# Optimization experiments

Measured on AMD Instinct MI355X. Metric: run time of the kernel, lower is better.

Reference implementation:

```python
import jax, jax.numpy as jnp
import numpy as np
import math

EPS = 1e-5
L2_EPS = 1e-12  # torch F.normalize default eps


def _bitlinear(x, W):
    """BitNet b1.58-style BitLinear: ternary weights (per-tensor mean-abs scale)
    and per-token int8 absmax activation quantization. No bias.
    x: [..., in], W: [out, in] -> [..., out]
    """
    w_scale = jnp.clip(jnp.mean(jnp.abs(W)), EPS, None)
    W_q = jnp.clip(jnp.round(W / w_scale), -1.0, 1.0) * w_scale
    x_scale = 127.0 / jnp.clip(jnp.max(jnp.abs(x), axis=-1, keepdims=True), EPS, None)
    x_q = jnp.clip(jnp.round(x * x_scale), -128.0, 127.0) / x_scale
    return jnp.einsum('bsi,oi->bso', x_q, W_q)


def setup_inputs() -> dict:
    key = jax.random.key(0)
    k1, k2, k3 = jax.random.split(key, 3)
    B, S, D_in, P, D_out = 4, 4096, 2048, 16, 2048
    x = jax.random.normal(k1, (B, S, D_in), dtype=jnp.float32)
    # xavier_normal_: std = sqrt(2 / (fan_in + fan_out))
    Wk = jax.random.normal(k2, (P, D_in), dtype=jnp.float32) * math.sqrt(2.0 / (D_in + P))
    Wv = jax.random.normal(k3, (D_out, P), dtype=jnp.float32) * math.sqrt(2.0 / (P + D_out))
    return {"x": x, "Wk": Wk, "Wv": Wv}


def reference(x, Wk, Wv):
    # key projection -> [B, S, P]
    attn = _bitlinear(x, Wk)
    # gelu (exact erf form, torch default) + L2-normalize * sqrt(P)
    attn = jax.nn.gelu(attn, approximate=False)
    norm = jnp.clip(jnp.linalg.norm(attn, axis=-1, keepdims=True), L2_EPS, None)
    attn = attn / norm * jnp.sqrt(jnp.float32(attn.shape[-1]))
    # value projection -> [B, S, D_out]
    return _bitlinear(attn, Wv)
```

## Files before the change

kernel.cpp:

```cpp
#include <hip/hip_runtime.h>
#include <hip/hip_bf16.h>

#define DIN   2048
#define DOUT  2048
#define NP    16
#define TPW   8

#define HDR_OFF   0
#define PART_OFF  64
#define WK4_OFF   256
#define WV4_OFF   (WK4_OFF + 32768)
#define Q2_OFF    (WV4_OFF + 32768)

static __device__ __forceinline__ int dot4(unsigned a, unsigned b, int c) {
#if defined(__has_builtin) && __has_builtin(__builtin_amdgcn_sdot4)
  return __builtin_amdgcn_sdot4((int)a, (int)b, c, false);
#else
  c += (int)(signed char)(a & 0xffu)        * (int)(signed char)(b & 0xffu);
  c += (int)(signed char)((a >> 8) & 0xffu) * (int)(signed char)((b >> 8) & 0xffu);
  c += (int)(signed char)((a >> 16) & 0xffu)* (int)(signed char)((b >> 16) & 0xffu);
  c += (int)(signed char)(a >> 24)          * (int)(signed char)(b >> 24);
  return c;
#endif
}

static __device__ __forceinline__ unsigned qmagic(float f, float xs) {
  return __float_as_uint(fmaf(f, xs, 12582912.0f)) & 0xffu;
}

static __device__ __forceinline__ unsigned q8(float f, float xs) {
  float t = f * xs;
  float r = rintf(t);
  r = fmaxf(-128.0f, fminf(127.0f, r));
  return ((unsigned)(int)r) & 0xffu;
}

__global__ __launch_bounds__(256) void k_reduce(
    const float* __restrict__ Wk, const float* __restrict__ Wv,
    float* __restrict__ partials)
{
  __shared__ float red[256];
  const int tid = threadIdx.x, b = blockIdx.x;
  const float4* W = (const float4*)((b < 8) ? Wk : Wv);
  const int lb = b & 7;

  float s = 0.f;
#pragma unroll
  for (int i = 0; i < 4; ++i) {
    float4 v = W[lb * 1024 + i * 256 + tid];
    s += fabsf(v.x) + fabsf(v.y) + fabsf(v.z) + fabsf(v.w);
  }
  red[tid] = s;
  __syncthreads();
  for (int o = 128; o > 0; o >>= 1) {
    if (tid < o) red[tid] += red[tid + o];
    __syncthreads();
  }
  if (tid == 0) partials[b] = red[0];
}

__global__ __launch_bounds__(256) void k_pack(
    const float* __restrict__ Wk, const float* __restrict__ Wv,
    const float* __restrict__ partials, float* __restrict__ hdr,
    unsigned* __restrict__ wk4, unsigned* __restrict__ wv4)
{
  const int tid = threadIdx.x, b = blockIdx.x;
  const int isV = (b >= 32);
  float sum = 0.f;
#pragma unroll
  for (int i = 0; i < 8; ++i) sum += partials[isV * 8 + i];
  const float sc = fmaxf(sum * (1.0f / 32768.0f), 1e-5f);
  if (tid == 0 && (b == 0 || b == 32)) hdr[isV] = sc;

  if (!isV) {
    const int c = b * 256 + tid;
    float4 w = ((const float4*)Wk)[c];
    unsigned pk = 0;
    const float* wp = &w.x;
#pragma unroll
    for (int j = 0; j < 4; ++j) {
      float r = rintf(wp[j] / sc);
      r = fmaxf(-1.0f, fminf(1.0f, r));
      pk |= (((unsigned)(int)r) & 0xffu) << (8 * j);
    }
    wk4[c] = pk;
  } else {
    const int o = (b - 32) * 256 + tid;
    unsigned u[4];
#pragma unroll
    for (int c = 0; c < 4; ++c) {
      float4 w = ((const float4*)Wv)[o * 4 + c];
      const float* wp = &w.x;
      unsigned pk = 0;
#pragma unroll
      for (int r = 0; r < 4; ++r) {
        float q = rintf(wp[r] / sc);
        q = fmaxf(-1.0f, fminf(1.0f, q));
        pk |= (((unsigned)(int)q) & 0xffu) << (8 * r);
      }
      u[c] = pk;
    }
    ((uint4*)wv4)[o] = make_uint4(u[0], u[1], u[2], u[3]);
  }
}

__global__ __launch_bounds__(64, 2) void kA(
    const float* __restrict__ x, const float* __restrict__ hdr,
    const unsigned* __restrict__ wk4, uint4* __restrict__ q2w, float* __restrict__ s2w)
{
  const int l = threadIdx.x;
  const long t0 = (long)blockIdx.x * TPW;
  const float w1 = hdr[0], w2 = hdr[1];

  unsigned wk[16][8];
#pragma unroll
  for (int p = 0; p < 16; ++p)
#pragma unroll
    for (int c = 0; c < 8; ++c) wk[p][c] = wk4[p * 512 + c * 64 + l];

  const float4* xf = (const float4*)x;

  int   svi[4];
  float s1v[4];

  for (int i = 0; i < TPW; ++i) {
    const long tok = t0 + i;

    float4 a[8];
#pragma unroll
    for (int c = 0; c < 8; ++c) a[c] = xf[tok * 512 + c * 64 + l];

    float mx = 0.0f;
#pragma unroll
    for (int c = 0; c < 8; ++c) {
      mx = fmaxf(mx, fabsf(a[c].x)); mx = fmaxf(mx, fabsf(a[c].y));
      mx = fmaxf(mx, fabsf(a[c].z)); mx = fmaxf(mx, fabsf(a[c].w));
    }
#pragma unroll
    for (int d = 1; d < 64; d <<= 1) mx = fmaxf(mx, __shfl_xor(mx, d, 64));
    const float mcl = fmaxf(mx, 1e-5f);
    const float xs = 127.0f / mcl;
    s1v[i & 3] = w1 / xs;

    unsigned qp[8];
#pragma unroll
    for (int c = 0; c < 8; ++c) {
      qp[c] = qmagic(a[c].x, xs) | (qmagic(a[c].y, xs) << 8)
            | (qmagic(a[c].z, xs) << 16) | (qmagic(a[c].w, xs) << 24);
    }

    int acc[16];
#pragma unroll
    for (int p = 0; p < 16; ++p) {
      int d = 0;
#pragma unroll
      for (int c = 0; c < 8; ++c) d = dot4(qp[c], wk[p][c], d);
      acc[p] = d;
    }

#pragma unroll
    for (int b = 0; b < 4; ++b) {
      const int lb = (l >> b) & 1;
#pragma unroll
      for (int j = 0; j < 8; ++j) {
        if (j < (8 >> b)) {
          int keep = lb ? acc[2 * j + 1] : acc[2 * j];
          int send = lb ? acc[2 * j]     : acc[2 * j + 1];
          acc[j] = keep + __shfl_xor(send, 1 << b, 64);
        }
      }
    }
    svi[i & 3] = acc[0];

    if ((i & 3) == 3) {
      const int lb4 = (l >> 4) & 1, lb5 = (l >> 5) & 1;
      int r0 = (lb4 ? svi[1] : svi[0]) + __shfl_xor(lb4 ? svi[0] : svi[1], 16, 64);
      int r1 = (lb4 ? svi[3] : svi[2]) + __shfl_xor(lb4 ? svi[2] : svi[3], 16, 64);
      int rr = (lb5 ? r1 : r0) + __shfl_xor(lb5 ? r0 : r1, 32, 64);
      float s1a = lb4 ? s1v[1] : s1v[0];
      float s1b = lb4 ? s1v[3] : s1v[2];
      const float s1sel = lb5 ? s1b : s1a;

      const float fa = (float)rr * s1sel;
      const float gv = 0.5f * fa * (1.0f + erff(fa * 0.70710678118654752f));
      float ss = gv * gv;
      ss += __shfl_xor(ss, 1, 64); ss += __shfl_xor(ss, 2, 64);
      ss += __shfl_xor(ss, 4, 64); ss += __shfl_xor(ss, 8, 64);
      const float rn = fmaxf(sqrtf(ss), 1e-12f);
      const float gn = gv * (4.0f / rn);
      float am = fabsf(gn);
      {
        float o;
        o = __shfl_xor(am, 1, 64); am = fmaxf(am, o);
        o = __shfl_xor(am, 2, 64); am = fmaxf(am, o);
        o = __shfl_xor(am, 4, 64); am = fmaxf(am, o);
        o = __shfl_xor(am, 8, 64); am = fmaxf(am, o);
      }
      const float mc2 = fmaxf(am, 1e-5f);
      const float xs2 = 127.0f / mc2;
      const float s2 = w2 / xs2;

      unsigned sh = q8(gn, xs2) << ((l & 3) * 8);
      sh |= (unsigned)__shfl_xor((int)sh, 1, 64);
      sh |= (unsigned)__shfl_xor((int)sh, 2, 64);
      const unsigned wa = (unsigned)__shfl_xor((int)sh, 4, 64);
      const unsigned wb = (unsigned)__shfl_xor((int)sh, 8, 64);
      const unsigned wc = (unsigned)__shfl_xor((int)sh, 12, 64);
      if ((l & 15) == 0) {
        const long tk = t0 + (i & ~3) + (l >> 4);
        q2w[tk] = make_uint4(sh, wa, wb, wc);
        s2w[tk] = s2;
      }
    }
  }
}

__global__ __launch_bounds__(64, 2) void kB(
    const uint4* __restrict__ wv4, const uint4* __restrict__ q2w,
    const float* __restrict__ s2w, float* __restrict__ out)
{
  const int l = threadIdx.x;
  const long t0 = (long)blockIdx.x * TPW;

  uint4 wv[8][4];
#pragma unroll
  for (int m = 0; m < 8; ++m)
#pragma unroll
    for (int j = 0; j < 4; ++j) wv[m][j] = wv4[m * 256 + l * 4 + j];

  for (int i = 0; i < TPW; ++i) {
    const long tok = t0 + i;
    const uint4 q = q2w[tok];
    const float s2 = s2w[tok];
#pragma unroll
    for (int m = 0; m < 8; ++m) {
      float h[4];
#pragma unroll
      for (int j = 0; j < 4; ++j) {
        int d = dot4(q.x, wv[m][j].x, 0);
        d = dot4(q.y, wv[m][j].y, d);
        d = dot4(q.z, wv[m][j].z, d);
        d = dot4(q.w, wv[m][j].w, d);
        h[j] = (float)d * s2;
      }
      *(float4*)(out + (size_t)tok * 2048 + m * 256 + l * 4) =
          make_float4(h[0], h[1], h[2], h[3]);
    }
  }
}

extern "C" void kernel_launch(void* const* d_in, const int* in_sizes, int n_in,
                              void* d_out, int out_size, void* d_ws, size_t ws_size,
                              hipStream_t stream) {
  const float* x  = (const float*)d_in[0];
  const float* Wk = (const float*)d_in[1];
  const float* Wv = (const float*)d_in[2];

  const int tokens = in_sizes[0] / DIN;

  char* ws = (char*)d_ws;
  float*    hdr  = (float*)(ws + HDR_OFF);
  float*    part = (float*)(ws + PART_OFF);
  unsigned* wk4  = (unsigned*)(ws + WK4_OFF);
  unsigned* wv4  = (unsigned*)(ws + WV4_OFF);
  uint4*    q2w  = (uint4*)(ws + Q2_OFF);
  float*    s2w  = (float*)(ws + Q2_OFF + (size_t)tokens * 16);

  k_reduce<<<16, 256, 0, stream>>>(Wk, Wv, part);
  k_pack<<<40, 256, 0, stream>>>(Wk, Wv, part, hdr, wk4, wv4);
  kA<<<tokens / TPW, 64, 0, stream>>>(x, hdr, wk4, q2w, s2w);
  kB<<<tokens / TPW, 64, 0, stream>>>((const uint4*)wv4, q2w, s2w, (float*)d_out);
}
```

Before: 254.1 us.

## Fuse key and value projection kernels and merge weight prep kernels

```diff
diff --git a/kernel.cpp b/kernel.cpp
--- a/kernel.cpp
+++ b/kernel.cpp
@@ -1,16 +1,14 @@
 #include <hip/hip_runtime.h>
-#include <hip/hip_bf16.h>
 
 #define DIN   2048
 #define DOUT  2048
 #define NP    16
 #define TPW   8
+#define WPB   2
 
 #define HDR_OFF   0
-#define PART_OFF  64
 #define WK4_OFF   256
 #define WV4_OFF   (WK4_OFF + 32768)
-#define Q2_OFF    (WV4_OFF + 32768)
 
 static __device__ __forceinline__ int dot4(unsigned a, unsigned b, int c) {
 #if defined(__has_builtin) && __has_builtin(__builtin_amdgcn_sdot4)
@@ -35,48 +33,45 @@
   return ((unsigned)(int)r) & 0xffu;
 }
 
-__global__ __launch_bounds__(256) void k_reduce(
+__global__ __launch_bounds__(256) void k_prep(
     const float* __restrict__ Wk, const float* __restrict__ Wv,
-    float* __restrict__ partials)
+    float* __restrict__ hdr, unsigned* __restrict__ wk4, unsigned* __restrict__ wv4)
 {
-  __shared__ float red[256];
-  const int tid = threadIdx.x, b = blockIdx.x;
-  const float4* W = (const float4*)((b < 8) ? Wk : Wv);
-  const int lb = b & 7;
-
-  float s = 0.f;
-#pragma unroll
-  for (int i = 0; i < 4; ++i) {
-    float4 v = W[lb * 1024 + i * 256 + tid];
-    s += fabsf(v.x) + fabsf(v.y) + fabsf(v.z) + fabsf(v.w);
-  }
-  red[tid] = s;
-  __syncthreads();
-  for (int o = 128; o > 0; o >>= 1) {
-    if (tid < o) red[tid] += red[tid + o];
-    __syncthreads();
-  }
-  if (tid == 0) partials[b] = red[0];
-}
-
-__global__ __launch_bounds__(256) void k_pack(
-    const float* __restrict__ Wk, const float* __restrict__ Wv,
-    const float* __restrict__ partials, float* __restrict__ hdr,
-    unsigned* __restrict__ wk4, unsigned* __restrict__ wv4)
-{
+  __shared__ float red[8][256];
   const int tid = threadIdx.x, b = blockIdx.x;
   const int isV = (b >= 32);
+  const float4* W = (const float4*)(isV ? Wv : Wk);
+
+  float4 own = make_float4(0.f, 0.f, 0.f, 0.f);
+#pragma unroll
+  for (int lb = 0; lb < 8; ++lb) {
+    float s = 0.f;
+#pragma unroll
+    for (int i = 0; i < 4; ++i) {
+      float4 v = W[lb * 1024 + i * 256 + tid];
+      if (!isV && (lb * 4 + i) == b) own = v;
+      s += fabsf(v.x) + fabsf(v.y) + fabsf(v.z) + fabsf(v.w);
+    }
+    red[lb][tid] = s;
+  }
+  __syncthreads();
+#pragma unroll 1
+  for (int o = 128; o > 0; o >>= 1) {
+    if (tid < o) {
+#pragma unroll
+      for (int lb = 0; lb < 8; ++lb) red[lb][tid] += red[lb][tid + o];
+    }
+    __syncthreads();
+  }
   float sum = 0.f;
 #pragma unroll
-  for (int i = 0; i < 8; ++i) sum += partials[isV * 8 + i];
+  for (int lb = 0; lb < 8; ++lb) sum += red[lb][0];
   const float sc = fmaxf(sum * (1.0f / 32768.0f), 1e-5f);
   if (tid == 0 && (b == 0 || b == 32)) hdr[isV] = sc;
 
   if (!isV) {
     const int c = b * 256 + tid;
-    float4 w = ((const float4*)Wk)[c];
-    unsigned pk = 0;
-    const float* wp = &w.x;
+    unsigned pk = 0; const float* wp = &own.x;
 #pragma unroll
     for (int j = 0; j < 4; ++j) {
       float r = rintf(wp[j] / sc);
@@ -88,8 +83,8 @@
     const int o = (b - 32) * 256 + tid;
     unsigned u[4];
 #pragma unroll
-    for (int c = 0; c < 4; ++c) {
-      float4 w = ((const float4*)Wv)[o * 4 + c];
+    for (int cc = 0; cc < 4; ++cc) {
+      float4 w = ((const float4*)Wv)[o * 4 + cc];
       const float* wp = &w.x;
       unsigned pk = 0;
 #pragma unroll
@@ -98,149 +93,159 @@
         q = fmaxf(-1.0f, fminf(1.0f, q));
         pk |= (((unsigned)(int)q) & 0xffu) << (8 * r);
       }
-      u[c] = pk;
+      u[cc] = pk;
     }
     ((uint4*)wv4)[o] = make_uint4(u[0], u[1], u[2], u[3]);
   }
 }
 
-__global__ __launch_bounds__(64, 2) void kA(
+__global__ __launch_bounds__(128, 2) void k_main(
     const float* __restrict__ x, const float* __restrict__ hdr,
-    const unsigned* __restrict__ wk4, uint4* __restrict__ q2w, float* __restrict__ s2w)
+    const unsigned* __restrict__ wk4, const unsigned* __restrict__ wv4,
+    float* __restrict__ out)
 {
-  const int l = threadIdx.x;
-  const long t0 = (long)blockIdx.x * TPW;
+  const int l  = threadIdx.x & 63;
+  const int ws = threadIdx.x >> 6;
+  const long t0 = ((long)blockIdx.x * WPB + ws) * TPW;
+
+  __shared__ uint4 qls[WPB][TPW];
+  __shared__ float sls[WPB][TPW];
+
   const float w1 = hdr[0], w2 = hdr[1];
-
-  unsigned wk[16][8];
+  const float4* xf = (const float4*)x;
+
+  unsigned tab[128];
 #pragma unroll
   for (int p = 0; p < 16; ++p)
 #pragma unroll
-    for (int c = 0; c < 8; ++c) wk[p][c] = wk4[p * 512 + c * 64 + l];
-
-  const float4* xf = (const float4*)x;
-
-  int   svi[4];
-  float s1v[4];
+    for (int c = 0; c < 8; ++c) tab[p * 8 + c] = wk4[p * 512 + c * 64 + l];
+
+  float4 a[2][8];
+#pragma unroll
+  for (int c = 0; c < 8; ++c) a[0][c] = xf[t0 * 512 + c * 64 + l];
+
+#pragma unroll 1
+  for (int g = 0; g < TPW / 4; ++g) {
+    int   sv[4];
+    float s1[4];
+#pragma unroll
+    for (int ii = 0; ii < 4; ++ii) {
+      const long tok = t0 + g * 4 + ii;
+
+      float mx = 0.0f;
+#pragma unroll
+      for (int c = 0; c < 8; ++c) {
+        float4 v = a[ii & 1][c];
+        mx = fmaxf(mx, fabsf(v.x)); mx = fmaxf(mx, fabsf(v.y));
+        mx = fmaxf(mx, fabsf(v.z)); mx = fmaxf(mx, fabsf(v.w));
+      }
+#pragma unroll
+      for (int d = 1; d < 64; d <<= 1) mx = fmaxf(mx, __shfl_xor(mx, d, 64));
+      const float mcl = fmaxf(mx, 1e-5f);
+      const float xs  = 127.0f / mcl;
+      s1[ii] = w1 / xs;
+
+      unsigned qp[8];
+#pragma unroll
+      for (int c = 0; c < 8; ++c) {
+        float4 v = a[ii & 1][c];
+        qp[c] = qmagic(v.x, xs) | (qmagic(v.y, xs) << 8)
+              | (qmagic(v.z, xs) << 16) | (qmagic(v.w, xs) << 24);
+      }
+
+      if (g * 4 + ii < TPW - 1) {
+#pragma unroll
+        for (int c = 0; c < 8; ++c)
+          a[(ii + 1) & 1][c] = xf[(tok + 1) * 512 + c * 64 + l];
+      }
+
+      int acc[16];
+#pragma unroll
+      for (int p = 0; p < 16; ++p) {
+        int d = 0;
+#pragma unroll
+        for (int c = 0; c < 8; ++c) d = dot4(qp[c], tab[p * 8 + c], d);
+        acc[p] = d;
+      }
+
+#pragma unroll
+      for (int b = 0; b < 4; ++b) {
+        const int lb = (l >> b) & 1;
+#pragma unroll
+        for (int j = 0; j < 8; ++j) {
+          if (j < (8 >> b)) {
+            int keep = lb ? acc[2 * j + 1] : acc[2 * j];
+            int send = lb ? acc[2 * j]     : acc[2 * j + 1];
+            acc[j] = keep + __shfl_xor(send, 1 << b, 64);
+          }
+        }
+      }
+      sv[ii] = acc[0];
+    }
+
+    const int lb4 = (l >> 4) & 1, lb5 = (l >> 5) & 1;
+    int r0 = (lb4 ? sv[1] : sv[0]) + __shfl_xor(lb4 ? sv[0] : sv[1], 16, 64);
+    int r1 = (lb4 ? sv[3] : sv[2]) + __shfl_xor(lb4 ? sv[2] : sv[3], 16, 64);
+    int rr = (lb5 ? r1 : r0) + __shfl_xor(lb5 ? r0 : r1, 32, 64);
+    float s1a = lb4 ? s1[1] : s1[0];
+    float s1b = lb4 ? s1[3] : s1[2];
+    const float s1sel = lb5 ? s1b : s1a;
+
+    const float fa = (float)rr * s1sel;
+    const float gv = 0.5f * fa * (1.0f + erff(fa * 0.70710678118654752f));
+    float ss = gv * gv;
+    ss += __shfl_xor(ss, 1, 64); ss += __shfl_xor(ss, 2, 64);
+    ss += __shfl_xor(ss, 4, 64); ss += __shfl_xor(ss, 8, 64);
+    const float rn = fmaxf(sqrtf(ss), 1e-12f);
+    const float gn = gv * (4.0f / rn);
+    float am = fabsf(gn);
+    {
+      float o;
+      o = __shfl_xor(am, 1, 64); am = fmaxf(am, o);
+      o = __shfl_xor(am, 2, 64); am = fmaxf(am, o);
+      o = __shfl_xor(am, 4, 64); am = fmaxf(am, o);
+      o = __shfl_xor(am, 8, 64); am = fmaxf(am, o);
+    }
+    const float mc2 = fmaxf(am, 1e-5f);
+    const float xs2 = 127.0f / mc2;
+    const float s2  = w2 / xs2;
+
+    unsigned sh = q8(gn, xs2) << ((l & 3) * 8);
+    sh |= (unsigned)__shfl_xor((int)sh, 1, 64);
+    sh |= (unsigned)__shfl_xor((int)sh, 2, 64);
+    const unsigned wa = (unsigned)__shfl_xor((int)sh, 4, 64);
+    const unsigned wb = (unsigned)__shfl_xor((int)sh, 8, 64);
+    const unsigned wc = (unsigned)__shfl_xor((int)sh, 12, 64);
+    if ((l & 15) == 0) {
+      qls[ws][g * 4 + (l >> 4)] = make_uint4(sh, wa, wb, wc);
+      sls[ws][g * 4 + (l >> 4)] = s2;
+    }
+  }
+
+#pragma unroll
+  for (int m = 0; m < 8; ++m)
+#pragma unroll
+    for (int j = 0; j < 4; ++j) {
+      uint4 t = ((const uint4*)wv4)[m * 256 + l * 4 + j];
+      tab[(m * 4 + j) * 4 + 0] = t.x; tab[(m * 4 + j) * 4 + 1] = t.y;
+      tab[(m * 4 + j) * 4 + 2] = t.z; tab[(m * 4 + j) * 4 + 3] = t.w;
+    }
+
+  __syncthreads();
 
   for (int i = 0; i < TPW; ++i) {
     const long tok = t0 + i;
-
-    float4 a[8];
-#pragma unroll
-    for (int c = 0; c < 8; ++c) a[c] = xf[tok * 512 + c * 64 + l];
-
-    float mx = 0.0f;
-#pragma unroll
-    for (int c = 0; c < 8; ++c) {
-      mx = fmaxf(mx, fabsf(a[c].x)); mx = fmaxf(mx, fabsf(a[c].y));
-      mx = fmaxf(mx, fabsf(a[c].z)); mx = fmaxf(mx, fabsf(a[c].w));
-    }
-#pragma unroll
-    for (int d = 1; d < 64; d <<= 1) mx = fmaxf(mx, __shfl_xor(mx, d, 64));
-    const float mcl = fmaxf(mx, 1e-5f);
-    const float xs = 127.0f / mcl;
-    s1v[i & 3] = w1 / xs;
-
-    unsigned qp[8];
-#pragma unroll
-    for (int c = 0; c < 8; ++c) {
-      qp[c] = qmagic(a[c].x, xs) | (qmagic(a[c].y, xs) << 8)
-            | (qmagic(a[c].z, xs) << 16) | (qmagic(a[c].w, xs) << 24);
-    }
-
-    int acc[16];
-#pragma unroll
-    for (int p = 0; p < 16; ++p) {
-      int d = 0;
-#pragma unroll
-      for (int c = 0; c < 8; ++c) d = dot4(qp[c], wk[p][c], d);
-      acc[p] = d;
-    }
-
-#pragma unroll
-    for (int b = 0; b < 4; ++b) {
-      const int lb = (l >> b) & 1;
-#pragma unroll
-      for (int j = 0; j < 8; ++j) {
-        if (j < (8 >> b)) {
-          int keep = lb ? acc[2 * j + 1] : acc[2 * j];
-          int send = lb ? acc[2 * j]     : acc[2 * j + 1];
-          acc[j] = keep + __shfl_xor(send, 1 << b, 64);
-        }
-      }
-    }
-    svi[i & 3] = acc[0];
-
-    if ((i & 3) == 3) {
-      const int lb4 = (l >> 4) & 1, lb5 = (l >> 5) & 1;
-      int r0 = (lb4 ? svi[1] : svi[0]) + __shfl_xor(lb4 ? svi[0] : svi[1], 16, 64);
-      int r1 = (lb4 ? svi[3] : svi[2]) + __shfl_xor(lb4 ? svi[2] : svi[3], 16, 64);
-      int rr = (lb5 ? r1 : r0) + __shfl_xor(lb5 ? r0 : r1, 32, 64);
-      float s1a = lb4 ? s1v[1] : s1v[0];
-      float s1b = lb4 ? s1v[3] : s1v[2];
-      const float s1sel = lb5 ? s1b : s1a;
-
-      const float fa = (float)rr * s1sel;
-      const float gv = 0.5f * fa * (1.0f + erff(fa * 0.70710678118654752f));
-      float ss = gv * gv;
-      ss += __shfl_xor(ss, 1, 64); ss += __shfl_xor(ss, 2, 64);
-      ss += __shfl_xor(ss, 4, 64); ss += __shfl_xor(ss, 8, 64);
-      const float rn = fmaxf(sqrtf(ss), 1e-12f);
-      const float gn = gv * (4.0f / rn);
-      float am = fabsf(gn);
-      {
-        float o;
-        o = __shfl_xor(am, 1, 64); am = fmaxf(am, o);
-        o = __shfl_xor(am, 2, 64); am = fmaxf(am, o);
-        o = __shfl_xor(am, 4, 64); am = fmaxf(am, o);
-        o = __shfl_xor(am, 8, 64); am = fmaxf(am, o);
-      }
-      const float mc2 = fmaxf(am, 1e-5f);
-      const float xs2 = 127.0f / mc2;
-      const float s2 = w2 / xs2;
-
-      unsigned sh = q8(gn, xs2) << ((l & 3) * 8);
-      sh |= (unsigned)__shfl_xor((int)sh, 1, 64);
-      sh |= (unsigned)__shfl_xor((int)sh, 2, 64);
-      const unsigned wa = (unsigned)__shfl_xor((int)sh, 4, 64);
-      const unsigned wb = (unsigned)__shfl_xor((int)sh, 8, 64);
-      const unsigned wc = (unsigned)__shfl_xor((int)sh, 12, 64);
-      if ((l & 15) == 0) {
-        const long tk = t0 + (i & ~3) + (l >> 4);
-        q2w[tk] = make_uint4(sh, wa, wb, wc);
-        s2w[tk] = s2;
-      }
-    }
-  }
-}
-
-__global__ __launch_bounds__(64, 2) void kB(
-    const uint4* __restrict__ wv4, const uint4* __restrict__ q2w,
-    const float* __restrict__ s2w, float* __restrict__ out)
-{
-  const int l = threadIdx.x;
-  const long t0 = (long)blockIdx.x * TPW;
-
-  uint4 wv[8][4];
-#pragma unroll
-  for (int m = 0; m < 8; ++m)
-#pragma unroll
-    for (int j = 0; j < 4; ++j) wv[m][j] = wv4[m * 256 + l * 4 + j];
-
-  for (int i = 0; i < TPW; ++i) {
-    const long tok = t0 + i;
-    const uint4 q = q2w[tok];
-    const float s2 = s2w[tok];
+    const uint4 q  = qls[ws][i];
+    const float s2 = sls[ws][i];
 #pragma unroll
     for (int m = 0; m < 8; ++m) {
       float h[4];
 #pragma unroll
       for (int j = 0; j < 4; ++j) {
-        int d = dot4(q.x, wv[m][j].x, 0);
-        d = dot4(q.y, wv[m][j].y, d);
-        d = dot4(q.z, wv[m][j].z, d);
-        d = dot4(q.w, wv[m][j].w, d);
+        int d = dot4(q.x, tab[(m * 4 + j) * 4 + 0], 0);
+        d = dot4(q.y, tab[(m * 4 + j) * 4 + 1], d);
+        d = dot4(q.z, tab[(m * 4 + j) * 4 + 2], d);
+        d = dot4(q.w, tab[(m * 4 + j) * 4 + 3], d);
         h[j] = (float)d * s2;
       }
       *(float4*)(out + (size_t)tok * 2048 + m * 256 + l * 4) =
@@ -259,15 +264,10 @@
   const int tokens = in_sizes[0] / DIN;
 
   char* ws = (char*)d_ws;
-  float*    hdr  = (float*)(ws + HDR_OFF);
-  float*    part = (float*)(ws + PART_OFF);
-  unsigned* wk4  = (unsigned*)(ws + WK4_OFF);
-  unsigned* wv4  = (unsigned*)(ws + WV4_OFF);
-  uint4*    q2w  = (uint4*)(ws + Q2_OFF);
-  float*    s2w  = (float*)(ws + Q2_OFF + (size_t)tokens * 16);
-
-  k_reduce<<<16, 256, 0, stream>>>(Wk, Wv, part);
-  k_pack<<<40, 256, 0, stream>>>(Wk, Wv, part, hdr, wk4, wv4);
-  kA<<<tokens / TPW, 64, 0, stream>>>(x, hdr, wk4, q2w, s2w);
-  kB<<<tokens / TPW, 64, 0, stream>>>((const uint4*)wv4, q2w, s2w, (float*)d_out);
-}
+  float*    hdr = (float*)(ws + HDR_OFF);
+  unsigned* wk4 = (unsigned*)(ws + WK4_OFF);
+  unsigned* wv4 = (unsigned*)(ws + WV4_OFF);
+
+  k_prep<<<40, 256, 0, stream>>>(Wk, Wv, hdr, wk4, wv4);
+  k_main<<<tokens / (TPW * WPB), 128, 0, stream>>>(x, hdr, wk4, wv4, (float*)d_out);
+}
```

Result: faster. 248.9 us (-2.0%).
